# Kernel optimization log

Hardware: AMD Instinct MI355X
Metric: run time of the kernel (lower is better)

The kernel has to match this reference:

```python
import jax, jax.numpy as jnp
import numpy as np

X0, Y0 = -51.2, -51.2          # cfg.X_RANGE[0], cfg.Y_RANGE[0]
VOXEL = 0.2                    # cfg.VOXEL_SIZE
GRID_W, GRID_H = 512, 512      # cfg.GRID_W, cfg.GRID_H
EPS = 1e-5                     # BatchNorm eps
B, N, C_IN = 2, 250000, 5
C_OUT2 = 128                   # out_channels * 2


def setup_inputs() -> dict:
    key = jax.random.key(0)
    ks = jax.random.split(key, 12)
    # points: x,y in a box slightly larger than the BEV range so mask is exercised
    xy = jax.random.uniform(ks[0], (B, N, 2), minval=-55.0, maxval=55.0, dtype=jnp.float32)
    z = jax.random.uniform(ks[1], (B, N, 1), minval=-3.0, maxval=1.0, dtype=jnp.float32)
    it = jax.random.uniform(ks[2], (B, N, 2), dtype=jnp.float32)  # intensity, time
    points = jnp.concatenate([xy, z, it], axis=-1)

    def lin_w(k, fi, fo):
        return jax.random.normal(k, (fi, fo), dtype=jnp.float32) / np.float32(np.sqrt(fi))

    return {
        "points": points,
        "W1": lin_w(ks[3], C_IN + 3, 64), "b1": jnp.zeros((64,), jnp.float32),
        "g1": jnp.ones((64,), jnp.float32), "be1": jnp.zeros((64,), jnp.float32),
        "m1": 0.1 * jax.random.normal(ks[4], (64,), jnp.float32),
        "v1": jnp.ones((64,), jnp.float32) + 0.1 * jax.random.uniform(ks[5], (64,)),
        "W2": lin_w(ks[6], 64, 64), "b2": jnp.zeros((64,), jnp.float32),
        "g2": jnp.ones((64,), jnp.float32), "be2": jnp.zeros((64,), jnp.float32),
        "m2": 0.1 * jax.random.normal(ks[7], (64,), jnp.float32),
        "v2": jnp.ones((64,), jnp.float32) + 0.1 * jax.random.uniform(ks[8], (64,)),
        "W3": lin_w(ks[9], 64, C_OUT2), "b3": jnp.zeros((C_OUT2,), jnp.float32),
    }


def _bn(x, g, be, m, v):
    # eval-mode BatchNorm1d: per-channel affine normalize
    return (x - m) * jax.lax.rsqrt(v + EPS) * g + be


def _frame(pts, W1, b1, g1, be1, m1, v1, W2, b2, g2, be2, m2, v2, W3, b3):
    # pts: [N, 5]
    # torch .long() truncates toward zero; astype(int32) does the same
    x_idx = ((pts[:, 0] - X0) / VOXEL).astype(jnp.int32)
    y_idx = ((pts[:, 1] - Y0) / VOXEL).astype(jnp.int32)
    mask = (x_idx >= 0) & (x_idx < GRID_W) & (y_idx >= 0) & (y_idx < GRID_H)

    xc = x_idx.astype(pts.dtype) * VOXEL + (X0 + VOXEL / 2)
    yc = y_idx.astype(pts.dtype) * VOXEL + (Y0 + VOXEL / 2)
    # z_center == pts[:,2], so the third residual is exactly zero (faithful)
    pts_aug = jnp.concatenate(
        [pts,
         (pts[:, 0] - xc)[:, None],
         (pts[:, 1] - yc)[:, None],
         jnp.zeros_like(pts[:, 2])[:, None]], axis=1)  # [N, 8]

    h = jax.nn.relu(_bn(pts_aug @ W1 + b1, g1, be1, m1, v1))
    h = jax.nn.relu(_bn(h @ W2 + b2, g2, be2, m2, v2))
    feat = h @ W3 + b3  # [N, 128]

    n_cells = GRID_H * GRID_W
    # invalid points routed to dummy segment n_cells
    idx = jnp.where(mask, y_idx * GRID_W + x_idx, n_cells)
    last = jax.ops.segment_max(jnp.arange(N, dtype=jnp.int32), idx,
                               num_segments=n_cells + 1)[:n_cells]  # [HW]
    canvas = jnp.where(last[:, None] >= 0,
                       feat[jnp.maximum(last, 0)], 0.0)  # [HW, 128]
    return canvas.T.reshape(C_OUT2, GRID_H, GRID_W)


def reference(points, W1, b1, g1, be1, m1, v1, W2, b2, g2, be2, m2, v2, W3, b3):
    f = lambda pts: _frame(pts, W1, b1, g1, be1, m1, v1,
                           W2, b2, g2, be2, m2, v2, W3, b3)
    return jax.vmap(f)(points)  # [B, 128, GRID_H, GRID_W]
```

## Files before the change

kernel.cpp:

```cpp
#include <hip/hip_runtime.h>

typedef __attribute__((ext_vector_type(8))) __bf16 bf16x8;
typedef __attribute__((ext_vector_type(4))) float f32x4;

#define GRID_W 512
#define GRID_H 512
#define HW (GRID_W * GRID_H)
#define NPTS 250000
#define NB 2
#define NCELLS (NB * HW)
#define SCAT_BLOCKS ((NB * NPTS + 255) / 256)

__device__ __forceinline__ void cell_of(float x, float y, int& xi, int& yi) {
    xi = (int)__fmul_rn(__fadd_rn(x, 51.2f), 5.0f);
    yi = (int)__fmul_rn(__fadd_rn(y, 51.2f), 5.0f);
}

__global__ __launch_bounds__(256) void k_scat_prep(
    const float* __restrict__ pts, int* __restrict__ win,
    const float* __restrict__ W1, const float* __restrict__ b1,
    const float* __restrict__ g1, const float* __restrict__ be1,
    const float* __restrict__ m1, const float* __restrict__ v1,
    const float* __restrict__ W2, const float* __restrict__ b2,
    const float* __restrict__ g2, const float* __restrict__ be2,
    const float* __restrict__ m2, const float* __restrict__ v2,
    const float* __restrict__ W3, const float* __restrict__ b3,
    float* __restrict__ w1f, float* __restrict__ bb1,
    float* __restrict__ bb2, float* __restrict__ b3f,
    __bf16* __restrict__ w2hi, __bf16* __restrict__ w2lo,
    __bf16* __restrict__ w3hi, __bf16* __restrict__ w3lo)
{
    if (blockIdx.x < SCAT_BLOCKS) {
        int gid = blockIdx.x * 256 + threadIdx.x;
        if (gid >= NB * NPTS) return;
        int b = gid / NPTS;
        int i = gid - b * NPTS;
        const float* p = pts + (size_t)gid * 5;
        int xi, yi;
        cell_of(p[0], p[1], xi, yi);
        if (xi >= 0 && xi < GRID_W && yi >= 0 && yi < GRID_H) {
            atomicMax(&win[b * HW + yi * GRID_W + xi], i);
        }
        return;
    }
    int gid = (blockIdx.x - SCAT_BLOCKS) * 256 + threadIdx.x;
    if (gid < 64) {
        int t = gid;
        float s1 = g1[t] / sqrtf(v1[t] + 1e-5f);
        bb1[t] = (b1[t] - m1[t]) * s1 + be1[t];
        float s2 = g2[t] / sqrtf(v2[t] + 1e-5f);
        bb2[t] = (b2[t] - m2[t]) * s2 + be2[t];
    } else if (gid < 192) {
        b3f[gid - 64] = b3[gid - 64];
    } else if (gid < 704) {
        int e = gid - 192;
        int j = e & 63;
        float s1 = g1[j] / sqrtf(v1[j] + 1e-5f);
        w1f[e] = W1[e] * s1;
    } else if (gid < 4800) {
        int e = gid - 704;
        int j = e & 7, n = (e >> 3) & 15, g = (e >> 7) & 7, nt = e >> 10;
        int k = g * 8 + j, ng = nt * 16 + n;
        float s2 = g2[ng] / sqrtf(v2[ng] + 1e-5f);
        float wf = W2[k * 64 + ng] * s2;
        __bf16 hi = (__bf16)wf;
        w2hi[e] = hi;
        w2lo[e] = (__bf16)(wf - (float)hi);
    } else if (gid < 12992) {
        int e = gid - 4800;
        int j = e & 7, n = (e >> 3) & 15, g = (e >> 7) & 7, nt = e >> 10;
        int k = g * 8 + j, ng = nt * 16 + n;
        float wf = W3[k * 128 + ng];
        __bf16 hi = (__bf16)wf;
        w3hi[e] = hi;
        w3lo[e] = (__bf16)(wf - (float)hi);
    }
}

__global__ __launch_bounds__(256, 3) void k_mlp(
    const float* __restrict__ pts, const int* __restrict__ win,
    const float* __restrict__ w1f, const float* __restrict__ bb1,
    const float* __restrict__ bb2, const float* __restrict__ b3f,
    const __bf16* __restrict__ w2hi, const __bf16* __restrict__ w2lo,
    const __bf16* __restrict__ w3hi, const __bf16* __restrict__ w3lo,
    float* __restrict__ out)
{
    __shared__ float sW1f[512];
    __shared__ float sBB1[64], sBB2[64], sB3[128];
    __shared__ float sMask[256];
    __shared__ __bf16 sAhi[4][4096];
    __shared__ float sT[4][16 * 68];

    const int t = threadIdx.x;
    const int wv = t >> 6;
    const int lane = t & 63;

    const int bI = blockIdx.x >> 10;
    const int cellBase = (blockIdx.x & 1023) * 256;
    const int gcell = bI * HW + cellBase + t;

    int w = win[gcell];
    sMask[t] = (w >= 0) ? 1.0f : 0.0f;

    float px = 0.f, py = 0.f, pz = 0.f, pin = 0.f, ptm = 0.f;
    if (w >= 0) {
        const float* p = pts + ((size_t)bI * NPTS + w) * 5;
        px = p[0]; py = p[1]; pz = p[2]; pin = p[3]; ptm = p[4];
    }

    if (t < 128)      ((float4*)sW1f)[t]       = ((const float4*)w1f)[t];
    else if (t < 144) ((float4*)sBB1)[t - 128] = ((const float4*)bb1)[t - 128];
    else if (t < 160) ((float4*)sBB2)[t - 144] = ((const float4*)bb2)[t - 144];
    else if (t < 192) ((float4*)sB3)[t - 160]  = ((const float4*)b3f)[t - 160];
    __syncthreads();

    float a8[8];
    a8[0] = px; a8[1] = py; a8[2] = pz; a8[3] = pin; a8[4] = ptm;
    {
        int xi, yi;
        cell_of(px, py, xi, yi);
        float xc = __fadd_rn(__fmul_rn((float)xi, 0.2f), -51.1f);
        float yc = __fadd_rn(__fmul_rn((float)yi, 0.2f), -51.1f);
        a8[5] = __fadd_rn(px, -xc);
        a8[6] = __fadd_rn(py, -yc);
        a8[7] = 0.0f;
    }
    float h1[64];
#pragma unroll
    for (int j4 = 0; j4 < 16; ++j4) {
        float4 acc = ((const float4*)sBB1)[j4];
#pragma unroll
        for (int k = 0; k < 8; ++k) {
            float4 wq = ((const float4*)sW1f)[k * 16 + j4];
            acc.x = fmaf(a8[k], wq.x, acc.x);
            acc.y = fmaf(a8[k], wq.y, acc.y);
            acc.z = fmaf(a8[k], wq.z, acc.z);
            acc.w = fmaf(a8[k], wq.w, acc.w);
        }
        h1[j4 * 4 + 0] = fmaxf(acc.x, 0.0f);
        h1[j4 * 4 + 1] = fmaxf(acc.y, 0.0f);
        h1[j4 * 4 + 2] = fmaxf(acc.z, 0.0f);
        h1[j4 * 4 + 3] = fmaxf(acc.w, 0.0f);
    }

    {
        int abase = (lane >> 4) * 1024 + (lane & 15) * 8;
#pragma unroll
        for (int g = 0; g < 8; ++g) {
            bf16x8 hi8;
#pragma unroll
            for (int j = 0; j < 8; ++j)
                hi8[j] = (__bf16)h1[g * 8 + j];
            *(bf16x8*)&sAhi[wv][abase + g * 128] = hi8;
        }
    }

    bf16x8 Ahi[4][2];
#pragma unroll
    for (int mt = 0; mt < 4; ++mt)
#pragma unroll
        for (int ks = 0; ks < 2; ++ks)
            Ahi[mt][ks] = *(const bf16x8*)&sAhi[wv][mt * 1024 + ks * 512 + lane * 8];

#pragma unroll
    for (int nt = 0; nt < 4; ++nt) {
        bf16x8 Bhi[2], Blo[2];
#pragma unroll
        for (int ks = 0; ks < 2; ++ks) {
            int off = nt * 1024 + ks * 512 + lane * 8;
            Bhi[ks] = *(const bf16x8*)&w2hi[off];
            Blo[ks] = *(const bf16x8*)&w2lo[off];
        }
        f32x4 zero = {0.f, 0.f, 0.f, 0.f};
        f32x4 acc[4] = {zero, zero, zero, zero};
#pragma unroll
        for (int mt = 0; mt < 4; ++mt)
#pragma unroll
            for (int ks = 0; ks < 2; ++ks) {
                acc[mt] = __builtin_amdgcn_mfma_f32_16x16x32_bf16(Ahi[mt][ks], Bhi[ks], acc[mt], 0, 0, 0);
                acc[mt] = __builtin_amdgcn_mfma_f32_16x16x32_bf16(Ahi[mt][ks], Blo[ks], acc[mt], 0, 0, 0);
            }
        float bb2l = sBB2[nt * 16 + (lane & 15)];
        int gg = nt * 2 + ((lane & 15) >> 3);
        int jj = lane & 7;
#pragma unroll
        for (int mt = 0; mt < 4; ++mt)
#pragma unroll
            for (int r = 0; r < 4; ++r) {
                float h = fmaxf(acc[mt][r] + bb2l, 0.0f);
                int off = mt * 1024 + gg * 128 + ((lane >> 4) * 4 + r) * 8 + jj;
                sAhi[wv][off] = (__bf16)h;
            }
    }

#pragma unroll
    for (int mt = 0; mt < 4; ++mt)
#pragma unroll
        for (int ks = 0; ks < 2; ++ks)
            Ahi[mt][ks] = *(const bf16x8*)&sAhi[wv][mt * 1024 + ks * 512 + lane * 8];

    float4 mk[4];
#pragma unroll
    for (int mt = 0; mt < 4; ++mt)
        mk[mt] = *(const float4*)&sMask[wv * 64 + mt * 16 + (lane >> 4) * 4];

    float* outW = out + (size_t)bI * 128 * HW + cellBase + wv * 64;
    float* sTw = sT[wv];
    const int g = lane >> 4;
    const int ch = lane & 15;
#pragma unroll
    for (int nt = 0; nt < 8; ++nt) {
        bf16x8 Bhi[2], Blo[2];
#pragma unroll
        for (int ks = 0; ks < 2; ++ks) {
            int off = nt * 1024 + ks * 512 + lane * 8;
            Bhi[ks] = *(const bf16x8*)&w3hi[off];
            Blo[ks] = *(const bf16x8*)&w3lo[off];
        }
        f32x4 zero = {0.f, 0.f, 0.f, 0.f};
        f32x4 acc[4] = {zero, zero, zero, zero};
#pragma unroll
        for (int mt = 0; mt < 4; ++mt)
#pragma unroll
            for (int ks = 0; ks < 2; ++ks) {
                acc[mt] = __builtin_amdgcn_mfma_f32_16x16x32_bf16(Ahi[mt][ks], Bhi[ks], acc[mt], 0, 0, 0);
                acc[mt] = __builtin_amdgcn_mfma_f32_16x16x32_bf16(Ahi[mt][ks], Blo[ks], acc[mt], 0, 0, 0);
            }
        float b3l = sB3[nt * 16 + ch];

#pragma unroll
        for (int mt = 0; mt < 4; ++mt) {
            f32x4 o;
            o[0] = (acc[mt][0] + b3l) * mk[mt].x;
            o[1] = (acc[mt][1] + b3l) * mk[mt].y;
            o[2] = (acc[mt][2] + b3l) * mk[mt].z;
            o[3] = (acc[mt][3] + b3l) * mk[mt].w;
            *(f32x4*)&sTw[ch * 68 + mt * 16 + g * 4] = o;
        }
#pragma unroll
        for (int j = 0; j < 4; ++j) {
            int chl = j * 4 + g;
            f32x4 v = *(const f32x4*)&sTw[chl * 68 + ch * 4];
            *(f32x4*)(outW + (size_t)(nt * 16 + chl) * HW + ch * 4) = v;
        }
    }
}

extern "C" void kernel_launch(void* const* d_in, const int* in_sizes, int n_in,
                              void* d_out, int out_size, void* d_ws, size_t ws_size,
                              hipStream_t stream) {
    const float* pts = (const float*)d_in[0];
    const float* W1  = (const float*)d_in[1];
    const float* b1  = (const float*)d_in[2];
    const float* g1  = (const float*)d_in[3];
    const float* be1 = (const float*)d_in[4];
    const float* m1  = (const float*)d_in[5];
    const float* v1  = (const float*)d_in[6];
    const float* W2  = (const float*)d_in[7];
    const float* b2  = (const float*)d_in[8];
    const float* g2  = (const float*)d_in[9];
    const float* be2 = (const float*)d_in[10];
    const float* m2  = (const float*)d_in[11];
    const float* v2  = (const float*)d_in[12];
    const float* W3  = (const float*)d_in[13];
    const float* b3  = (const float*)d_in[14];
    float* out = (float*)d_out;

    char* wsb = (char*)d_ws;
    int*    win  = (int*)wsb;
    float*  w1f  = (float*)(wsb + 2097152);
    float*  bb1  = (float*)(wsb + 2097152 + 2048);
    float*  bb2  = (float*)(wsb + 2097152 + 2304);
    float*  b3f  = (float*)(wsb + 2097152 + 2560);
    __bf16* w2hi = (__bf16*)(wsb + 2097152 + 3072);
    __bf16* w2lo = w2hi + 4096;
    __bf16* w3hi = w2lo + 4096;
    __bf16* w3lo = w3hi + 8192;

    hipMemsetAsync(win, 0xFF, (size_t)NCELLS * sizeof(int), stream);
    k_scat_prep<<<SCAT_BLOCKS + 51, 256, 0, stream>>>(pts, win,
        W1, b1, g1, be1, m1, v1,
        W2, b2, g2, be2, m2, v2, W3, b3,
        w1f, bb1, bb2, b3f, w2hi, w2lo, w3hi, w3lo);
    k_mlp<<<NCELLS / 256, 256, 0, stream>>>(pts, win,
        w1f, bb1, bb2, b3f, w2hi, w2lo, w3hi, w3lo, out);
}
```

Before: 87.43 us.

## Process two 256-cell tiles per block and build mask from wave ballot

Each k_mlp block now handles 512 cells in two sequential 256-cell passes, halving the grid. Shared weights and biases are staged once per two tiles, and both tiles' point gathers are issued up front so their latency overlaps. The shared-memory mask array is replaced by wave ballots, with each lane extracting its mask bits from registers. The cost is fewer blocks in flight, more registers live across the loop, and possible loss of occupancy on a kernel bound by output writes.

```diff
diff --git a/kernel.cpp b/kernel.cpp
--- a/kernel.cpp
+++ b/kernel.cpp
@@ -87,7 +87,6 @@
 {
     __shared__ float sW1f[512];
     __shared__ float sBB1[64], sBB2[64], sB3[128];
-    __shared__ float sMask[256];
     __shared__ __bf16 sAhi[4][4096];
     __shared__ float sT[4][16 * 68];
 
@@ -95,17 +94,27 @@
     const int wv = t >> 6;
     const int lane = t & 63;
 
-    const int bI = blockIdx.x >> 10;
-    const int cellBase = (blockIdx.x & 1023) * 256;
+    const int bI = blockIdx.x >> 9;
+    const int cellBase = (blockIdx.x & 511) * 512;
     const int gcell = bI * HW + cellBase + t;
 
-    int w = win[gcell];
-    sMask[t] = (w >= 0) ? 1.0f : 0.0f;
-
-    float px = 0.f, py = 0.f, pz = 0.f, pin = 0.f, ptm = 0.f;
-    if (w >= 0) {
-        const float* p = pts + ((size_t)bI * NPTS + w) * 5;
-        px = p[0]; py = p[1]; pz = p[2]; pin = p[3]; ptm = p[4];
+    int w0 = win[gcell];
+    int w1 = win[gcell + 256];
+    unsigned long long mb[2];
+    mb[0] = __ballot(w0 >= 0);
+    mb[1] = __ballot(w1 >= 0);
+    float P[2][5];
+#pragma unroll
+    for (int tl = 0; tl < 2; ++tl)
+#pragma unroll
+        for (int c = 0; c < 5; ++c) P[tl][c] = 0.0f;
+    if (w0 >= 0) {
+        const float* p = pts + ((size_t)bI * NPTS + w0) * 5;
+        P[0][0] = p[0]; P[0][1] = p[1]; P[0][2] = p[2]; P[0][3] = p[3]; P[0][4] = p[4];
+    }
+    if (w1 >= 0) {
+        const float* p = pts + ((size_t)bI * NPTS + w1) * 5;
+        P[1][0] = p[0]; P[1][1] = p[1]; P[1][2] = p[2]; P[1][3] = p[3]; P[1][4] = p[4];
     }
 
     if (t < 128)      ((float4*)sW1f)[t]       = ((const float4*)w1f)[t];
@@ -114,134 +123,144 @@
     else if (t < 192) ((float4*)sB3)[t - 160]  = ((const float4*)b3f)[t - 160];
     __syncthreads();
 
-    float a8[8];
-    a8[0] = px; a8[1] = py; a8[2] = pz; a8[3] = pin; a8[4] = ptm;
-    {
-        int xi, yi;
-        cell_of(px, py, xi, yi);
-        float xc = __fadd_rn(__fmul_rn((float)xi, 0.2f), -51.1f);
-        float yc = __fadd_rn(__fmul_rn((float)yi, 0.2f), -51.1f);
-        a8[5] = __fadd_rn(px, -xc);
-        a8[6] = __fadd_rn(py, -yc);
-        a8[7] = 0.0f;
-    }
-    float h1[64];
-#pragma unroll
-    for (int j4 = 0; j4 < 16; ++j4) {
-        float4 acc = ((const float4*)sBB1)[j4];
-#pragma unroll
-        for (int k = 0; k < 8; ++k) {
-            float4 wq = ((const float4*)sW1f)[k * 16 + j4];
-            acc.x = fmaf(a8[k], wq.x, acc.x);
-            acc.y = fmaf(a8[k], wq.y, acc.y);
-            acc.z = fmaf(a8[k], wq.z, acc.z);
-            acc.w = fmaf(a8[k], wq.w, acc.w);
-        }
-        h1[j4 * 4 + 0] = fmaxf(acc.x, 0.0f);
-        h1[j4 * 4 + 1] = fmaxf(acc.y, 0.0f);
-        h1[j4 * 4 + 2] = fmaxf(acc.z, 0.0f);
-        h1[j4 * 4 + 3] = fmaxf(acc.w, 0.0f);
-    }
-
-    {
-        int abase = (lane >> 4) * 1024 + (lane & 15) * 8;
-#pragma unroll
-        for (int g = 0; g < 8; ++g) {
-            bf16x8 hi8;
-#pragma unroll
-            for (int j = 0; j < 8; ++j)
-                hi8[j] = (__bf16)h1[g * 8 + j];
-            *(bf16x8*)&sAhi[wv][abase + g * 128] = hi8;
-        }
-    }
-
-    bf16x8 Ahi[4][2];
-#pragma unroll
-    for (int mt = 0; mt < 4; ++mt)
-#pragma unroll
-        for (int ks = 0; ks < 2; ++ks)
-            Ahi[mt][ks] = *(const bf16x8*)&sAhi[wv][mt * 1024 + ks * 512 + lane * 8];
-
-#pragma unroll
-    for (int nt = 0; nt < 4; ++nt) {
-        bf16x8 Bhi[2], Blo[2];
-#pragma unroll
-        for (int ks = 0; ks < 2; ++ks) {
-            int off = nt * 1024 + ks * 512 + lane * 8;
-            Bhi[ks] = *(const bf16x8*)&w2hi[off];
-            Blo[ks] = *(const bf16x8*)&w2lo[off];
-        }
-        f32x4 zero = {0.f, 0.f, 0.f, 0.f};
-        f32x4 acc[4] = {zero, zero, zero, zero};
-#pragma unroll
-        for (int mt = 0; mt < 4; ++mt)
-#pragma unroll
-            for (int ks = 0; ks < 2; ++ks) {
-                acc[mt] = __builtin_amdgcn_mfma_f32_16x16x32_bf16(Ahi[mt][ks], Bhi[ks], acc[mt], 0, 0, 0);
-                acc[mt] = __builtin_amdgcn_mfma_f32_16x16x32_bf16(Ahi[mt][ks], Blo[ks], acc[mt], 0, 0, 0);
-            }
-        float bb2l = sBB2[nt * 16 + (lane & 15)];
-        int gg = nt * 2 + ((lane & 15) >> 3);
-        int jj = lane & 7;
-#pragma unroll
-        for (int mt = 0; mt < 4; ++mt)
-#pragma unroll
-            for (int r = 0; r < 4; ++r) {
-                float h = fmaxf(acc[mt][r] + bb2l, 0.0f);
-                int off = mt * 1024 + gg * 128 + ((lane >> 4) * 4 + r) * 8 + jj;
-                sAhi[wv][off] = (__bf16)h;
-            }
-    }
-
-#pragma unroll
-    for (int mt = 0; mt < 4; ++mt)
-#pragma unroll
-        for (int ks = 0; ks < 2; ++ks)
-            Ahi[mt][ks] = *(const bf16x8*)&sAhi[wv][mt * 1024 + ks * 512 + lane * 8];
-
-    float4 mk[4];
-#pragma unroll
-    for (int mt = 0; mt < 4; ++mt)
-        mk[mt] = *(const float4*)&sMask[wv * 64 + mt * 16 + (lane >> 4) * 4];
-
-    float* outW = out + (size_t)bI * 128 * HW + cellBase + wv * 64;
-    float* sTw = sT[wv];
     const int g = lane >> 4;
     const int ch = lane & 15;
-#pragma unroll
-    for (int nt = 0; nt < 8; ++nt) {
-        bf16x8 Bhi[2], Blo[2];
-#pragma unroll
-        for (int ks = 0; ks < 2; ++ks) {
-            int off = nt * 1024 + ks * 512 + lane * 8;
-            Bhi[ks] = *(const bf16x8*)&w3hi[off];
-            Blo[ks] = *(const bf16x8*)&w3lo[off];
-        }
-        f32x4 zero = {0.f, 0.f, 0.f, 0.f};
-        f32x4 acc[4] = {zero, zero, zero, zero};
+    float* sTw = sT[wv];
+
+#pragma unroll
+    for (int tl = 0; tl < 2; ++tl) {
+        float a8[8];
+        a8[0] = P[tl][0]; a8[1] = P[tl][1]; a8[2] = P[tl][2];
+        a8[3] = P[tl][3]; a8[4] = P[tl][4];
+        {
+            int xi, yi;
+            cell_of(a8[0], a8[1], xi, yi);
+            float xc = __fadd_rn(__fmul_rn((float)xi, 0.2f), -51.1f);
+            float yc = __fadd_rn(__fmul_rn((float)yi, 0.2f), -51.1f);
+            a8[5] = __fadd_rn(a8[0], -xc);
+            a8[6] = __fadd_rn(a8[1], -yc);
+            a8[7] = 0.0f;
+        }
+        float h1[64];
+#pragma unroll
+        for (int j4 = 0; j4 < 16; ++j4) {
+            float4 acc = ((const float4*)sBB1)[j4];
+#pragma unroll
+            for (int k = 0; k < 8; ++k) {
+                float4 wq = ((const float4*)sW1f)[k * 16 + j4];
+                acc.x = fmaf(a8[k], wq.x, acc.x);
+                acc.y = fmaf(a8[k], wq.y, acc.y);
+                acc.z = fmaf(a8[k], wq.z, acc.z);
+                acc.w = fmaf(a8[k], wq.w, acc.w);
+            }
+            h1[j4 * 4 + 0] = fmaxf(acc.x, 0.0f);
+            h1[j4 * 4 + 1] = fmaxf(acc.y, 0.0f);
+            h1[j4 * 4 + 2] = fmaxf(acc.z, 0.0f);
+            h1[j4 * 4 + 3] = fmaxf(acc.w, 0.0f);
+        }
+
+        {
+            int abase = g * 1024 + ch * 8;
+#pragma unroll
+            for (int gg = 0; gg < 8; ++gg) {
+                bf16x8 hi8;
+#pragma unroll
+                for (int j = 0; j < 8; ++j)
+                    hi8[j] = (__bf16)h1[gg * 8 + j];
+                *(bf16x8*)&sAhi[wv][abase + gg * 128] = hi8;
+            }
+        }
+
+        bf16x8 Ahi[4][2];
 #pragma unroll
         for (int mt = 0; mt < 4; ++mt)
 #pragma unroll
+            for (int ks = 0; ks < 2; ++ks)
+                Ahi[mt][ks] = *(const bf16x8*)&sAhi[wv][mt * 1024 + ks * 512 + lane * 8];
+
+#pragma unroll
+        for (int nt = 0; nt < 4; ++nt) {
+            bf16x8 Bhi[2], Blo[2];
+#pragma unroll
             for (int ks = 0; ks < 2; ++ks) {
-                acc[mt] = __builtin_amdgcn_mfma_f32_16x16x32_bf16(Ahi[mt][ks], Bhi[ks], acc[mt], 0, 0, 0);
-                acc[mt] = __builtin_amdgcn_mfma_f32_16x16x32_bf16(Ahi[mt][ks], Blo[ks], acc[mt], 0, 0, 0);
-            }
-        float b3l = sB3[nt * 16 + ch];
-
+                int off = nt * 1024 + ks * 512 + lane * 8;
+                Bhi[ks] = *(const bf16x8*)&w2hi[off];
+                Blo[ks] = *(const bf16x8*)&w2lo[off];
+            }
+            f32x4 zero = {0.f, 0.f, 0.f, 0.f};
+            f32x4 acc[4] = {zero, zero, zero, zero};
+#pragma unroll
+            for (int mt = 0; mt < 4; ++mt)
+#pragma unroll
+                for (int ks = 0; ks < 2; ++ks) {
+                    acc[mt] = __builtin_amdgcn_mfma_f32_16x16x32_bf16(Ahi[mt][ks], Bhi[ks], acc[mt], 0, 0, 0);
+                    acc[mt] = __builtin_amdgcn_mfma_f32_16x16x32_bf16(Ahi[mt][ks], Blo[ks], acc[mt], 0, 0, 0);
+                }
+            float bb2l = sBB2[nt * 16 + ch];
+            int gg = nt * 2 + (ch >> 3);
+            int jj = lane & 7;
+#pragma unroll
+            for (int mt = 0; mt < 4; ++mt)
+#pragma unroll
+                for (int r = 0; r < 4; ++r) {
+                    float h = fmaxf(acc[mt][r] + bb2l, 0.0f);
+                    int off = mt * 1024 + gg * 128 + (g * 4 + r) * 8 + jj;
+                    sAhi[wv][off] = (__bf16)h;
+                }
+        }
+
+#pragma unroll
+        for (int mt = 0; mt < 4; ++mt)
+#pragma unroll
+            for (int ks = 0; ks < 2; ++ks)
+                Ahi[mt][ks] = *(const bf16x8*)&sAhi[wv][mt * 1024 + ks * 512 + lane * 8];
+
+        float4 mk[4];
 #pragma unroll
         for (int mt = 0; mt < 4; ++mt) {
-            f32x4 o;
-            o[0] = (acc[mt][0] + b3l) * mk[mt].x;
-            o[1] = (acc[mt][1] + b3l) * mk[mt].y;
-            o[2] = (acc[mt][2] + b3l) * mk[mt].z;
-            o[3] = (acc[mt][3] + b3l) * mk[mt].w;
-            *(f32x4*)&sTw[ch * 68 + mt * 16 + g * 4] = o;
-        }
-#pragma unroll
-        for (int j = 0; j < 4; ++j) {
-            int chl = j * 4 + g;
-            f32x4 v = *(const f32x4*)&sTw[chl * 68 + ch * 4];
-            *(f32x4*)(outW + (size_t)(nt * 16 + chl) * HW + ch * 4) = v;
+            int base = mt * 16 + g * 4;
+            mk[mt].x = ((mb[tl] >> (base + 0)) & 1ull) ? 1.0f : 0.0f;
+            mk[mt].y = ((mb[tl] >> (base + 1)) & 1ull) ? 1.0f : 0.0f;
+            mk[mt].z = ((mb[tl] >> (base + 2)) & 1ull) ? 1.0f : 0.0f;
+            mk[mt].w = ((mb[tl] >> (base + 3)) & 1ull) ? 1.0f : 0.0f;
+        }
+
+        float* outW = out + (size_t)bI * 128 * HW + cellBase + tl * 256 + wv * 64;
+#pragma unroll
+        for (int nt = 0; nt < 8; ++nt) {
+            bf16x8 Bhi[2], Blo[2];
+#pragma unroll
+            for (int ks = 0; ks < 2; ++ks) {
+                int off = nt * 1024 + ks * 512 + lane * 8;
+                Bhi[ks] = *(const bf16x8*)&w3hi[off];
+                Blo[ks] = *(const bf16x8*)&w3lo[off];
+            }
+            f32x4 zero = {0.f, 0.f, 0.f, 0.f};
+            f32x4 acc[4] = {zero, zero, zero, zero};
+#pragma unroll
+            for (int mt = 0; mt < 4; ++mt)
+#pragma unroll
+                for (int ks = 0; ks < 2; ++ks) {
+                    acc[mt] = __builtin_amdgcn_mfma_f32_16x16x32_bf16(Ahi[mt][ks], Bhi[ks], acc[mt], 0, 0, 0);
+                    acc[mt] = __builtin_amdgcn_mfma_f32_16x16x32_bf16(Ahi[mt][ks], Blo[ks], acc[mt], 0, 0, 0);
+                }
+            float b3l = sB3[nt * 16 + ch];
+
+#pragma unroll
+            for (int mt = 0; mt < 4; ++mt) {
+                f32x4 o;
+                o[0] = (acc[mt][0] + b3l) * mk[mt].x;
+                o[1] = (acc[mt][1] + b3l) * mk[mt].y;
+                o[2] = (acc[mt][2] + b3l) * mk[mt].z;
+                o[3] = (acc[mt][3] + b3l) * mk[mt].w;
+                *(f32x4*)&sTw[ch * 68 + mt * 16 + g * 4] = o;
+            }
+#pragma unroll
+            for (int j = 0; j < 4; ++j) {
+                int chl = j * 4 + g;
+                f32x4 v = *(const f32x4*)&sTw[chl * 68 + ch * 4];
+                *(f32x4*)(outW + (size_t)(nt * 16 + chl) * HW + ch * 4) = v;
+            }
         }
     }
 }
@@ -282,6 +301,6 @@
         W1, b1, g1, be1, m1, v1,
         W2, b2, g2, be2, m2, v2, W3, b3,
         w1f, bb1, bb2, b3f, w2hi, w2lo, w3hi, w3lo);
-    k_mlp<<<NCELLS / 256, 256, 0, stream>>>(pts, win,
+    k_mlp<<<NCELLS / 512, 256, 0, stream>>>(pts, win,
         w1f, bb1, bb2, b3f, w2hi, w2lo, w3hi, w3lo, out);
 }
```

Measured after the change: 112.6 us. +28.7%, slower.
